# Kernel optimization log

Hardware: AMD Instinct MI355X
Metric: run time of the kernel (lower is better)

The kernel has to match this reference:

```python
import jax, jax.numpy as jnp
import numpy as np

D_MODEL = 384
KSIZE = 3
B, L = 32, 512
LN_EPS = 1e-5


def _conv1d_same(x, w, b):
    # x: [B, C_in, L], w: [C_out, C_in, K] -> [B, C_out, L]
    y = jax.lax.conv_general_dilated(
        x, w, window_strides=(1,), padding='SAME',
        dimension_numbers=('NCH', 'OIH', 'NCH'))
    return y + b[None, :, None]


def _conv_fft_block(x, wa, ba, wb, bb):
    # Conv1D_FFT: transpose -> conv/relu -> conv/relu -> transpose back
    h = jnp.transpose(x, (0, 2, 1))            # [B, D, L]
    h = jax.nn.relu(_conv1d_same(h, wa, ba))
    h = jax.nn.relu(_conv1d_same(h, wb, bb))
    return jnp.transpose(h, (0, 2, 1))         # [B, L, D]


def _layernorm(x, g, b):
    mu = jnp.mean(x, axis=-1, keepdims=True)
    var = jnp.var(x, axis=-1, keepdims=True)
    return (x - mu) * jax.lax.rsqrt(var + LN_EPS) * g + b


def setup_inputs() -> dict:
    key = jax.random.key(0)
    ks = jax.random.split(key, 8)
    x = jax.random.normal(ks[0], (B, L, D_MODEL), dtype=jnp.float32)
    durations = jax.random.randint(ks[1], (B, L), 0, 8, dtype=jnp.int32)
    s = 0.02
    params = {
        'c1a_w': jax.random.normal(ks[2], (D_MODEL, D_MODEL, KSIZE), jnp.float32) * s,
        'c1a_b': jnp.zeros((D_MODEL,), jnp.float32),
        'c1b_w': jax.random.normal(ks[3], (D_MODEL, D_MODEL, KSIZE), jnp.float32) * s,
        'c1b_b': jnp.zeros((D_MODEL,), jnp.float32),
        'ln1_g': jnp.ones((D_MODEL,), jnp.float32),
        'ln1_b': jnp.zeros((D_MODEL,), jnp.float32),
        'c2a_w': jax.random.normal(ks[4], (D_MODEL, D_MODEL, KSIZE), jnp.float32) * s,
        'c2a_b': jnp.zeros((D_MODEL,), jnp.float32),
        'c2b_w': jax.random.normal(ks[5], (D_MODEL, D_MODEL, KSIZE), jnp.float32) * s,
        'c2b_b': jnp.zeros((D_MODEL,), jnp.float32),
        'ln2_g': jnp.ones((D_MODEL,), jnp.float32),
        'ln2_b': jnp.zeros((D_MODEL,), jnp.float32),
        'lin_w': jax.random.normal(ks[6], (D_MODEL, 1), jnp.float32) * s,
        'lin_b': jnp.zeros((1,), jnp.float32),
    }
    return {'x': x, 'durations': durations, **params}


def reference(x, durations, c1a_w, c1a_b, c1b_w, c1b_b, ln1_g, ln1_b,
              c2a_w, c2a_b, c2b_w, c2b_b, ln2_g, ln2_b, lin_w, lin_b):
    # --- DurationPredictor (dropout = identity, eval mode) ---
    h = _conv_fft_block(x, c1a_w, c1a_b, c1b_w, c1b_b)
    h = _layernorm(h, ln1_g, ln1_b)
    h = _conv_fft_block(h, c2a_w, c2a_b, c2b_w, c2b_b)
    h = _layernorm(h, ln2_g, ln2_b)
    dur_preds = (h @ lin_w + lin_b)[..., 0]      # [B, L]

    # --- LR: duration-based expansion via one-hot alignment matmul ---
    total = jnp.sum(durations, axis=-1)          # [B]
    T = int(jnp.max(total))                      # concrete (durations are input data)
    cum = jnp.cumsum(durations, axis=-1)         # [B, L]
    t = jnp.arange(T, dtype=cum.dtype)           # [T]
    # frame t belongs to phoneme j s.t. cum[j-1] <= t < cum[j]
    idx = jax.vmap(lambda c: jnp.searchsorted(c, t, side='right'))(cum)  # [B, T]
    mask = (t[None, :] < total[:, None]).astype(x.dtype)                 # [B, T]
    align = jax.nn.one_hot(idx, x.shape[1], dtype=x.dtype) * mask[:, :, None]  # [B, T, L]
    out = jnp.einsum('btl,bld->btd', align, x)   # [B, T, D]
    return (out, dur_preds)
```

## Files before the change

kernel.cpp:

```cpp
#include <hip/hip_runtime.h>

#define B_   32
#define L_   512
#define D_   384
#define M_   (B_*L_)
#define KTOT (D_*3)
#define LDW  392
#define BROWS 82
#define BUFE (BROWS*LDW)

typedef __bf16 bf16x8 __attribute__((ext_vector_type(8)));
typedef float  floatx4 __attribute__((ext_vector_type(4)));

__global__ __launch_bounds__(256) void repack4_kernel(const float* __restrict__ wa,
                                                      const float* __restrict__ wb,
                                                      const float* __restrict__ wc,
                                                      const float* __restrict__ wd,
                                                      __bf16* __restrict__ oa,
                                                      __bf16* __restrict__ ob,
                                                      __bf16* __restrict__ oc,
                                                      __bf16* __restrict__ od)
{
    int idx = blockIdx.x * 256 + threadIdx.x;
    if (idx >= D_ * KTOT) return;
    const float* w; __bf16* o_;
    switch (blockIdx.y) {
        case 0:  w = wa; o_ = oa; break;
        case 1:  w = wb; o_ = ob; break;
        case 2:  w = wc; o_ = oc; break;
        default: w = wd; o_ = od; break;
    }
    int j  = idx & 7;
    int l  = (idx >> 3) & 63;
    int ct = idx >> 9;
    int c  = ct / 24;
    int t  = ct - c * 24;
    int o  = t * 16 + (l & 15);
    int kflat = c * 32 + (l >> 4) * 8 + j;
    int s  = kflat / D_;
    int i  = kflat - s * D_;
    o_[idx] = (__bf16)w[(o * D_ + i) * 3 + s];
}

__global__ __launch_bounds__(512, 1) void fused_predictor(
    const float* __restrict__ x,
    const __bf16* __restrict__ w1a, const float* __restrict__ b1a,
    const __bf16* __restrict__ w1b, const float* __restrict__ b1b,
    const float* __restrict__ g1,  const float* __restrict__ e1,
    const __bf16* __restrict__ w2a, const float* __restrict__ b2a,
    const __bf16* __restrict__ w2b, const float* __restrict__ b2b,
    const float* __restrict__ g2,  const float* __restrict__ e2,
    const float* __restrict__ lw,  const float* __restrict__ lb,
    float* __restrict__ out_dur)
{
    extern __shared__ char smem_raw[];
    __bf16* bufA = (__bf16*)smem_raw;
    __bf16* bufB = bufA + BUFE;
    float*  red1 = (float*)(bufB + BUFE);
    float*  red2 = red1 + BROWS * 8;
    float*  minv = red2 + BROWS * 8;

    const int m0 = blockIdx.x * 64;
    const int l0 = m0 & 511;
    const int b0 = m0 - l0;

    const int tid  = threadIdx.x;
    const int wave = tid >> 6;
    const int lane = tid & 63;
    const int quad = lane >> 4;
    const int lx   = lane & 15;
    const int ng   = wave & 3;
    const int mg   = wave >> 2;
    const int mtc  = mg ? 2 : 3;
    const int mtb  = mg ? 3 : 0;

    bf16x8 kz;
#pragma unroll
    for (int z = 0; z < 8; z++) kz[z] = (__bf16)0.f;

    for (int c = tid; c < BROWS * 48; c += 512) {
        int beta = c / 48, q = c - beta * 48;
        int l = l0 + beta - 9;
        bf16x8 v = kz;
        if ((unsigned)l < (unsigned)L_) {
            const float* xr = x + (size_t)(b0 + l) * D_ + q * 8;
            const float4 f0 = *(const float4*)xr;
            const float4 f1 = *(const float4*)(xr + 4);
            v[0] = (__bf16)f0.x; v[1] = (__bf16)f0.y; v[2] = (__bf16)f0.z; v[3] = (__bf16)f0.w;
            v[4] = (__bf16)f1.x; v[5] = (__bf16)f1.y; v[6] = (__bf16)f1.z; v[7] = (__bf16)f1.w;
        }
        *(bf16x8*)(&bufA[beta * LDW + q * 8]) = v;
    }
    for (int c = tid; c < 2 * 48; c += 512) {
        int beta = (c < 48) ? 0 : 81, q = c % 48;
        *(bf16x8*)(&bufB[beta * LDW + q * 8]) = kz;
    }
    __syncthreads();

    const int t0   = ng * 6;
    const int col0 = ng * 96 + lx;

    floatx4 acc[3][6];
    bf16x8  bg[3][6];

    for (int st = 0; st < 4; st++) {
        const __bf16* bin  = (st & 1) ? bufB : bufA;
        __bf16*       bout = (st & 1) ? bufA : bufB;
        const __bf16* Wp = (st == 0) ? w1a : (st == 1) ? w1b : (st == 2) ? w2a : w2b;
        const float*  bp = (st == 0) ? b1a : (st == 1) ? b1b : (st == 2) ? b2a : b2b;

#pragma unroll
        for (int mt = 0; mt < 3; mt++)
            if (mt < mtc)
#pragma unroll
                for (int ni = 0; ni < 6; ni++)
#pragma unroll
                    for (int r = 0; r < 4; r++) acc[mt][ni][r] = 0.f;

        const char* pb0 = (const char*)Wp + ((size_t)t0 * 64 + lane) * 16;
        auto loadB = [&](int buf, int n) {
            int it = n / 3, s = n - it * 3;
            const char* p = pb0 + (size_t)(s * 12 + it) * 24576;
#pragma unroll
            for (int ni = 0; ni < 6; ni++)
                bg[buf][ni] = *(const bf16x8*)(p + ni * 1024);
        };
        loadB(0, 0); loadB(1, 1);

        const __bf16* ab = bin + (mtb * 16 + lx) * LDW + quad * 8;
#pragma unroll
        for (int n = 0; n < 36; n++) {
            const int it = n / 3, s = n - it * 3;
            if (n + 2 < 36) loadB((n + 2) % 3, n + 2);
            bf16x8 af[3];
            af[0] = *(const bf16x8*)(ab + (s) * LDW + it * 32);
            af[1] = *(const bf16x8*)(ab + (16 + s) * LDW + it * 32);
            if (mtc == 3)
                af[2] = *(const bf16x8*)(ab + (32 + s) * LDW + it * 32);
            __builtin_amdgcn_s_setprio(1);
#pragma unroll
            for (int ni = 0; ni < 6; ni++) {
                acc[0][ni] = __builtin_amdgcn_mfma_f32_16x16x32_bf16(af[0], bg[n % 3][ni], acc[0][ni], 0, 0, 0);
                acc[1][ni] = __builtin_amdgcn_mfma_f32_16x16x32_bf16(af[1], bg[n % 3][ni], acc[1][ni], 0, 0, 0);
            }
            if (mtc == 3) {
#pragma unroll
                for (int ni = 0; ni < 6; ni++)
                    acc[2][ni] = __builtin_amdgcn_mfma_f32_16x16x32_bf16(af[2], bg[n % 3][ni], acc[2][ni], 0, 0, 0);
            }
            __builtin_amdgcn_s_setprio(0);
        }

        float bv[6];
#pragma unroll
        for (int ni = 0; ni < 6; ni++) bv[ni] = bp[col0 + ni * 16];
#pragma unroll
        for (int mt = 0; mt < 3; mt++)
            if (mt < mtc)
#pragma unroll
                for (int ni = 0; ni < 6; ni++)
#pragma unroll
                    for (int r = 0; r < 4; r++) {
                        float vv = acc[mt][ni][r] + bv[ni];
                        acc[mt][ni][r] = vv > 0.f ? vv : 0.f;
                    }

        if (st == 1 || st == 3) {
#pragma unroll
            for (int mt = 0; mt < 3; mt++)
                if (mt < mtc)
#pragma unroll
                    for (int r = 0; r < 4; r++) {
                        float s1 = 0.f, s2 = 0.f;
#pragma unroll
                        for (int ni = 0; ni < 6; ni++) {
                            s1 += acc[mt][ni][r];
                            s2 += acc[mt][ni][r] * acc[mt][ni][r];
                        }
#pragma unroll
                        for (int d = 1; d < 16; d <<= 1) {
                            s1 += __shfl_xor(s1, d);
                            s2 += __shfl_xor(s2, d);
                        }
                        if (lx == 0) {
                            int beta = (mtb + mt) * 16 + quad * 4 + r + 1;
                            red1[beta * 8 + wave] = s1;
                            red2[beta * 8 + wave] = s2;
                        }
                    }
            __syncthreads();
            if (tid < BROWS) {
                int tile = (tid - 1) >> 4;
                int base = (tile >= 3) ? 4 : 0;
                float s1 = 0.f, s2 = 0.f;
#pragma unroll
                for (int k = 0; k < 4; k++) { s1 += red1[tid * 8 + base + k]; s2 += red2[tid * 8 + base + k]; }
                float mean = s1 * (1.f / D_);
                float var  = s2 * (1.f / D_) - mean * mean;
                minv[tid * 2]     = mean;
                minv[tid * 2 + 1] = rsqrtf(var + 1e-5f);
            }
            __syncthreads();
            const float* gp = (st == 1) ? g1 : g2;
            const float* ep = (st == 1) ? e1 : e2;
            float gv[6], ev[6];
#pragma unroll
            for (int ni = 0; ni < 6; ni++) { gv[ni] = gp[col0 + ni * 16]; ev[ni] = ep[col0 + ni * 16]; }
#pragma unroll
            for (int mt = 0; mt < 3; mt++)
                if (mt < mtc)
#pragma unroll
                    for (int r = 0; r < 4; r++) {
                        int beta = (mtb + mt) * 16 + quad * 4 + r + 1;
                        float mean = minv[beta * 2], inv = minv[beta * 2 + 1];
#pragma unroll
                        for (int ni = 0; ni < 6; ni++)
                            acc[mt][ni][r] = (acc[mt][ni][r] - mean) * inv * gv[ni] + ev[ni];
                    }
            if (st == 1) {
#pragma unroll
                for (int mt = 0; mt < 3; mt++)
                    if (mt < mtc)
#pragma unroll
                        for (int r = 0; r < 4; r++) {
                            int beta = (mtb + mt) * 16 + quad * 4 + r + 1;
                            bool ok = (unsigned)(l0 + beta - 9) < (unsigned)L_;
#pragma unroll
                            for (int ni = 0; ni < 6; ni++)
                                bout[beta * LDW + col0 + ni * 16] = (__bf16)(ok ? acc[mt][ni][r] : 0.f);
                        }
            } else {
                float lwv[6];
#pragma unroll
                for (int ni = 0; ni < 6; ni++) lwv[ni] = lw[col0 + ni * 16];
#pragma unroll
                for (int mt = 0; mt < 3; mt++)
                    if (mt < mtc)
#pragma unroll
                        for (int r = 0; r < 4; r++) {
                            float p = 0.f;
#pragma unroll
                            for (int ni = 0; ni < 6; ni++) p += acc[mt][ni][r] * lwv[ni];
#pragma unroll
                            for (int d = 1; d < 16; d <<= 1) p += __shfl_xor(p, d);
                            if (lx == 0) {
                                int beta = (mtb + mt) * 16 + quad * 4 + r + 1;
                                red1[beta * 8 + wave] = p;
                            }
                        }
                __syncthreads();
                if (tid < 64) {
                    int beta = tid + 9;
                    int tile = (beta - 1) >> 4;
                    int base = (tile >= 3) ? 4 : 0;
                    float sacc = lb[0];
#pragma unroll
                    for (int k = 0; k < 4; k++) sacc += red1[beta * 8 + base + k];
                    out_dur[m0 + tid] = sacc;
                }
            }
        } else {
#pragma unroll
            for (int mt = 0; mt < 3; mt++)
                if (mt < mtc)
#pragma unroll
                    for (int r = 0; r < 4; r++) {
                        int beta = (mtb + mt) * 16 + quad * 4 + r + 1;
                        bool ok = (unsigned)(l0 + beta - 9) < (unsigned)L_;
#pragma unroll
                        for (int ni = 0; ni < 6; ni++)
                            bout[beta * LDW + col0 + ni * 16] = (__bf16)(ok ? acc[mt][ni][r] : 0.f);
                    }
        }
        __syncthreads();
    }
}

__global__ __launch_bounds__(64) void cum_kernel(const int* __restrict__ dur,
                                                 int* __restrict__ cum)
{
    int b = blockIdx.x, lane = threadIdx.x;
    const int* db = dur + b * L_;
    int v[8], s = 0;
#pragma unroll
    for (int i = 0; i < 8; i++) { v[i] = db[lane * 8 + i]; s += v[i]; }
    int ex = s;
#pragma unroll
    for (int off = 1; off < 64; off <<= 1) {
        int n = __shfl_up(ex, off);
        if (lane >= off) ex += n;
    }
    ex -= s;
    int c = ex;
    int* cb = cum + b * L_;
#pragma unroll
    for (int i = 0; i < 8; i++) { c += v[i]; cb[lane * 8 + i] = c; }
}

__global__ __launch_bounds__(128) void gather_kernel(const float* __restrict__ x,
                                                     const int* __restrict__ cum,
                                                     float* __restrict__ out, int T)
{
    int fr = blockIdx.x;
    int b  = fr / T;
    int t  = fr - b * T;
    int tid = threadIdx.x;
    const int* cb = cum + b * L_;
    int total = cb[L_ - 1];
    float4 val = make_float4(0.f, 0.f, 0.f, 0.f);
    if (t < total) {
        int lo = 0, hi = L_;
        while (lo < hi) { int mid = (lo + hi) >> 1; if (cb[mid] > t) hi = mid; else lo = mid + 1; }
        if (tid < 96) val = *(const float4*)(x + ((size_t)(b * L_ + lo)) * D_ + tid * 4);
    }
    if (tid < 96) *(float4*)(out + (size_t)fr * D_ + tid * 4) = val;
}

extern "C" void kernel_launch(void* const* d_in, const int* in_sizes, int n_in,
                              void* d_out, int out_size, void* d_ws, size_t ws_size,
                              hipStream_t stream) {
    const float* x       = (const float*)d_in[0];
    const int*   dur     = (const int*)d_in[1];
    const float* c1a_w   = (const float*)d_in[2];
    const float* c1a_b   = (const float*)d_in[3];
    const float* c1b_w   = (const float*)d_in[4];
    const float* c1b_b   = (const float*)d_in[5];
    const float* ln1_g   = (const float*)d_in[6];
    const float* ln1_b   = (const float*)d_in[7];
    const float* c2a_w   = (const float*)d_in[8];
    const float* c2a_b   = (const float*)d_in[9];
    const float* c2b_w   = (const float*)d_in[10];
    const float* c2b_b   = (const float*)d_in[11];
    const float* ln2_g   = (const float*)d_in[12];
    const float* ln2_b   = (const float*)d_in[13];
    const float* lin_w   = (const float*)d_in[14];
    const float* lin_b   = (const float*)d_in[15];

    const int T = (out_size - B_ * L_) / (B_ * D_);
    float* out_gather = (float*)d_out;
    float* out_dur    = (float*)d_out + (size_t)B_ * T * D_;

    char* p = (char*)d_ws;
    __bf16* w1a = (__bf16*)p; p += (size_t)D_ * KTOT * 2;
    __bf16* w1b = (__bf16*)p; p += (size_t)D_ * KTOT * 2;
    __bf16* w2a = (__bf16*)p; p += (size_t)D_ * KTOT * 2;
    __bf16* w2b = (__bf16*)p; p += (size_t)D_ * KTOT * 2;
    int* cum = (int*)p; p += (size_t)B_ * L_ * 4;

    cum_kernel<<<B_, 64, 0, stream>>>(dur, cum);
    gather_kernel<<<B_ * T, 128, 0, stream>>>(x, cum, out_gather, T);

    dim3 rpgrid((D_ * KTOT + 255) / 256, 4);
    repack4_kernel<<<rpgrid, 256, 0, stream>>>(c1a_w, c1b_w, c2a_w, c2b_w, w1a, w1b, w2a, w2b);

    const size_t smem = (size_t)2 * BUFE * 2 + (BROWS * 8 * 2 + BROWS * 2) * 4;
    static bool attr_set = false;
    if (!attr_set) {
        hipFuncSetAttribute((const void*)fused_predictor,
                            hipFuncAttributeMaxDynamicSharedMemorySize, (int)smem);
        attr_set = true;
    }
    fused_predictor<<<256, 512, smem, stream>>>(
        x, w1a, c1a_b, w1b, c1b_b, ln1_g, ln1_b,
        w2a, c2a_b, w2b, c2b_b, ln2_g, ln2_b,
        lin_w, lin_b, out_dur);
}
```

Before: 251.9 us.

## Replace per-frame binary-search gather with per-phoneme scatter plus zero-tail kernel

The length-regulator expansion changes from one block per output frame, which binary-searched the cumulative durations, to one block per input phoneme that loads its row once and writes it to every frame it covers. A separate kernel zero-fills the padded frames past each batch's total length. This removes the search and the repeated reads of x, and launches fewer blocks (B*L instead of B*T). In exchange, work per block now depends on the duration values and an extra kernel launch is added.

```diff
diff --git a/kernel.cpp b/kernel.cpp
--- a/kernel.cpp
+++ b/kernel.cpp
@@ -297,23 +297,39 @@
     for (int i = 0; i < 8; i++) { c += v[i]; cb[lane * 8 + i] = c; }
 }
 
-__global__ __launch_bounds__(128) void gather_kernel(const float* __restrict__ x,
-                                                     const int* __restrict__ cum,
-                                                     float* __restrict__ out, int T)
-{
-    int fr = blockIdx.x;
-    int b  = fr / T;
-    int t  = fr - b * T;
+__global__ __launch_bounds__(128) void scatter_kernel(const float* __restrict__ x,
+                                                      const int* __restrict__ cum,
+                                                      float* __restrict__ out, int T)
+{
+    int pl = blockIdx.x;
+    int b  = pl >> 9;
+    int l  = pl & (L_ - 1);
+    const int* cb = cum + b * L_;
+    int e = cb[l];
+    int s = l ? cb[l - 1] : 0;
+    if (e == s) return;
     int tid = threadIdx.x;
-    const int* cb = cum + b * L_;
-    int total = cb[L_ - 1];
-    float4 val = make_float4(0.f, 0.f, 0.f, 0.f);
-    if (t < total) {
-        int lo = 0, hi = L_;
-        while (lo < hi) { int mid = (lo + hi) >> 1; if (cb[mid] > t) hi = mid; else lo = mid + 1; }
-        if (tid < 96) val = *(const float4*)(x + ((size_t)(b * L_ + lo)) * D_ + tid * 4);
-    }
-    if (tid < 96) *(float4*)(out + (size_t)fr * D_ + tid * 4) = val;
+    float4 v = make_float4(0.f, 0.f, 0.f, 0.f);
+    if (tid < 96) v = *(const float4*)(x + (size_t)pl * D_ + tid * 4);
+    float* ob = out + ((size_t)b * T) * D_ + tid * 4;
+    if (tid < 96)
+        for (int t = s; t < e; ++t)
+            *(float4*)(ob + (size_t)t * D_) = v;
+}
+
+__global__ __launch_bounds__(256) void ztail_kernel(const int* __restrict__ cum,
+                                                    float* __restrict__ out, int T)
+{
+    int b = blockIdx.y;
+    int total = cum[b * L_ + L_ - 1];
+    int nfr = T - total;
+    if (nfr <= 0) return;
+    float* base = out + ((size_t)b * T + total) * D_;
+    int n4 = nfr * 96;
+    for (int i = blockIdx.x * 256 + threadIdx.x; i < n4; i += gridDim.x * 256) {
+        int fr = i / 96, q = i - fr * 96;
+        *(float4*)(base + (size_t)fr * D_ + q * 4) = make_float4(0.f, 0.f, 0.f, 0.f);
+    }
 }
 
 extern "C" void kernel_launch(void* const* d_in, const int* in_sizes, int n_in,
@@ -348,7 +364,8 @@
     int* cum = (int*)p; p += (size_t)B_ * L_ * 4;
 
     cum_kernel<<<B_, 64, 0, stream>>>(dur, cum);
-    gather_kernel<<<B_ * T, 128, 0, stream>>>(x, cum, out_gather, T);
+    scatter_kernel<<<B_ * L_, 128, 0, stream>>>(x, cum, out_gather, T);
+    ztail_kernel<<<dim3(16, B_), 256, 0, stream>>>(cum, out_gather, T);
 
     dim3 rpgrid((D_ * KTOT + 255) / 256, 4);
     repack4_kernel<<<rpgrid, 256, 0, stream>>>(c1a_w, c1b_w, c2a_w, c2b_w, w1a, w1b, w2a, w2b);
```

Measured after the change: 249.7 us. No clear change (-0.9%).
